# Kernel tuning notes

Hardware: AMD Instinct MI355X
Metric: run time of the kernel (lower is better)

Reference implementation:

```python
import jax, jax.numpy as jnp
import numpy as np
import math

B, S, D_IN, D_OUT, H = 2, 2048, 1024, 1024, 16
HD = D_OUT // H


def setup_inputs() -> dict:
    key = jax.random.key(0)
    ks = jax.random.split(key, 6)
    scale = 0.02
    return {
        "x": jax.random.normal(ks[0], (B, S, D_IN), dtype=jnp.float32),
        "Wq": jax.random.normal(ks[1], (D_IN, D_OUT), dtype=jnp.float32) * scale,
        "Wk": jax.random.normal(ks[2], (D_IN, D_OUT), dtype=jnp.float32) * scale,
        "Wv": jax.random.normal(ks[3], (D_IN, D_OUT), dtype=jnp.float32) * scale,
        "Wo": jax.random.normal(ks[4], (D_OUT, D_OUT), dtype=jnp.float32) * scale,
        "bo": jax.random.normal(ks[5], (D_OUT,), dtype=jnp.float32) * scale,
    }


def reference(x, Wq, Wk, Wv, Wo, bo):
    b, n, _ = x.shape
    # project and split heads -> [b, h, n, hd]
    q = (x @ Wq).reshape(b, n, H, HD).transpose(0, 2, 1, 3)
    k = (x @ Wk).reshape(b, n, H, HD).transpose(0, 2, 1, 3)
    v = (x @ Wv).reshape(b, n, H, HD).transpose(0, 2, 1, 3)
    # materialized [b, h, n, n] scores with causal mask (as in original)
    scores = jnp.einsum('bhqd,bhkd->bhqk', q, k)
    causal = jnp.tril(jnp.ones((n, n), dtype=bool))  # True = keep
    scores = jnp.where(causal, scores, -jnp.inf)
    attn = jax.nn.softmax(scores / math.sqrt(HD), axis=-1)
    ctx = jnp.einsum('bhqk,bhkd->bhqd', attn, v)
    ctx = ctx.transpose(0, 2, 1, 3).reshape(b, n, D_OUT)
    return ctx @ Wo + bo
```

## Files before the change

kernel.cpp:

```cpp
#include <hip/hip_runtime.h>
#include <hip/hip_bf16.h>
#include <math.h>

typedef __bf16 v8bf __attribute__((ext_vector_type(8)));
typedef __bf16 v4bf __attribute__((ext_vector_type(4)));
typedef short  v4s  __attribute__((ext_vector_type(4)));
typedef float  v4f  __attribute__((ext_vector_type(4)));
typedef unsigned short u16;

static_assert(sizeof(v8bf) == 16, "v8bf must be 16B");

__device__ __forceinline__ u16 f2bf(float f) {
  __hip_bfloat16 h = __float2bfloat16(f);
  return *reinterpret_cast<u16*>(&h);
}
__device__ __forceinline__ v4f mfma16(v8bf a, v8bf b, v4f c) {
  return __builtin_amdgcn_mfma_f32_16x16x32_bf16(a, b, c, 0, 0, 0);
}
__device__ __forceinline__ v4f mfma16k16(v4bf a, v4bf b, v4f c) {
#if __has_builtin(__builtin_amdgcn_mfma_f32_16x16x16_bf16)
  return __builtin_amdgcn_mfma_f32_16x16x16_bf16(a, b, c, 0, 0, 0);
#else
  union { v4bf f; v4s s; } ua, ub;
  ua.f = a; ub.f = b;
  return __builtin_amdgcn_mfma_f32_16x16x16bf16_1k(ua.s, ub.s, c, 0, 0, 0);
#endif
}
__device__ __forceinline__ void async16(const u16* g, u16* l) {
  __builtin_amdgcn_global_load_lds(
      (__attribute__((address_space(1))) void*)(void*)g,
      (__attribute__((address_space(3))) void*)l, 16, 0, 0);
}

__global__ void prep(const float* __restrict__ x, const float* __restrict__ Wq,
                     const float* __restrict__ Wk, const float* __restrict__ Wv,
                     const float* __restrict__ Wo, u16* __restrict__ Wt,
                     u16* __restrict__ xb) {
  int tx = threadIdx.x, ty = threadIdx.y;
  if (blockIdx.z == 4) {
    int bid = blockIdx.y * 32 + blockIdx.x;
    int i = (bid * 1024 + ty * 32 + tx) * 4;
    float4 v = *(const float4*)(x + i);
    ushort4 o;
    o.x = f2bf(v.x); o.y = f2bf(v.y); o.z = f2bf(v.z); o.w = f2bf(v.w);
    *(ushort4*)(xb + i) = o;
    return;
  }
  __shared__ float tile[32][33];
  const float* src = (blockIdx.z == 0) ? Wq : (blockIdx.z == 1) ? Wk : (blockIdx.z == 2) ? Wv : Wo;
  int k0 = blockIdx.x * 32, n0 = blockIdx.y * 32;
  tile[ty][tx] = src[(size_t)(k0 + ty) * 1024 + n0 + tx];
  __syncthreads();
  Wt[(size_t)(blockIdx.z * 1024 + n0 + ty) * 1024 + k0 + tx] = f2bf(tile[tx][ty]);
}

__device__ __forceinline__ void gemm_core(const u16* __restrict__ A, const u16* __restrict__ Bt,
                                          u16* sA, u16* sB, v4f acc[4][4], int bm, int bn) {
  const int t = threadIdx.x;
  const int w = t >> 6, l = t & 63;
  const int quad = l >> 4, low = l & 15;
  const int wm = (w & 1) * 64, wn = (w >> 1) * 64;
  const int rowA = bm * 128 + w * 32 + (l >> 2);
  const int rowB = bn * 128 + w * 32 + (l >> 2);
  const int col8 = (l & 3) * 8;
  u16* la = sA + w * 1024;
  u16* lb = sB + w * 1024;

  for (int kb = 0; kb < 1024; kb += 32) {
    async16(A + (size_t)rowA * 1024 + kb + col8, la);
    async16(A + (size_t)(rowA + 16) * 1024 + kb + col8, la + 512);
    async16(Bt + (size_t)rowB * 1024 + kb + col8, lb);
    async16(Bt + (size_t)(rowB + 16) * 1024 + kb + col8, lb + 512);
    __syncthreads();
    v8bf af[4], bfr[4];
#pragma unroll
    for (int i = 0; i < 4; i++)
      af[i] = *(const v8bf*)(sA + (wm + i * 16 + low) * 32 + quad * 8);
#pragma unroll
    for (int j = 0; j < 4; j++)
      bfr[j] = *(const v8bf*)(sB + (wn + j * 16 + low) * 32 + quad * 8);
#pragma unroll
    for (int i = 0; i < 4; i++)
#pragma unroll
      for (int j = 0; j < 4; j++)
        acc[i][j] = mfma16(af[i], bfr[j], acc[i][j]);
    __syncthreads();
  }
}

__global__ __launch_bounds__(256) void gemm_qkv(const u16* __restrict__ xb,
                                                const u16* __restrict__ Wt,
                                                u16* __restrict__ Qb,
                                                u16* __restrict__ Kb,
                                                u16* __restrict__ Vt) {
  __shared__ __align__(16) u16 sA[128 * 32];
  __shared__ __align__(16) u16 sB[128 * 32];
  v4f acc[4][4] = {};
  const int bm = blockIdx.x, bn = blockIdx.y;
  gemm_core(xb, Wt, sA, sB, acc, bm, bn);
  const int t = threadIdx.x, w = t >> 6, l = t & 63, quad = l >> 4, low = l & 15;
  const int wm = (w & 1) * 64, wn = (w >> 1) * 64;
  const int zone = (bn * 128) >> 10;
  const float qsc = (zone == 0) ? 0.18033688011112042f : 1.0f;
#pragma unroll
  for (int i = 0; i < 4; i++) {
    int m0 = bm * 128 + wm + i * 16 + quad * 4;
#pragma unroll
    for (int j = 0; j < 4; j++) {
      int nn = (bn * 128 + wn + j * 16 + low) & 1023;
      if (zone == 0) {
#pragma unroll
        for (int r = 0; r < 4; r++)
          Qb[(size_t)(m0 + r) * 1024 + nn] = f2bf(acc[i][j][r] * qsc);
      } else if (zone == 1) {
#pragma unroll
        for (int r = 0; r < 4; r++)
          Kb[(size_t)(m0 + r) * 1024 + nn] = f2bf(acc[i][j][r]);
      } else {
        int bb = m0 >> 11, s = m0 & 2047;
#pragma unroll
        for (int r = 0; r < 4; r++)
          Vt[(size_t)(bb * 1024 + nn) * 2048 + s + r] = f2bf(acc[i][j][r]);
      }
    }
  }
}

__global__ __launch_bounds__(256) void gemm_out(const u16* __restrict__ ctx,
                                                const u16* __restrict__ Wt,
                                                const float* __restrict__ bo,
                                                float* __restrict__ out) {
  __shared__ __align__(16) u16 sA[128 * 32];
  __shared__ __align__(16) u16 sB[64 * 32];
  const u16* Bt = Wt + (size_t)3072 * 1024;
  v4f acc[4][2] = {};
  const int bm = blockIdx.x, bn = blockIdx.y;
  const int t = threadIdx.x, w = t >> 6, l = t & 63, quad = l >> 4, low = l & 15;
  const int wm = (w & 1) * 64, wn = (w >> 1) * 32;
  const int rowA = bm * 128 + w * 32 + (l >> 2);
  const int rowB = bn * 64 + w * 16 + (l >> 2);
  const int col8 = (l & 3) * 8;
  u16* la = sA + w * 1024;
  u16* lb = sB + w * 512;

  for (int kb = 0; kb < 1024; kb += 32) {
    async16(ctx + (size_t)rowA * 1024 + kb + col8, la);
    async16(ctx + (size_t)(rowA + 16) * 1024 + kb + col8, la + 512);
    async16(Bt + (size_t)rowB * 1024 + kb + col8, lb);
    __syncthreads();
    v8bf af[4], bfr[2];
#pragma unroll
    for (int i = 0; i < 4; i++)
      af[i] = *(const v8bf*)(sA + (wm + i * 16 + low) * 32 + quad * 8);
#pragma unroll
    for (int j = 0; j < 2; j++)
      bfr[j] = *(const v8bf*)(sB + (wn + j * 16 + low) * 32 + quad * 8);
#pragma unroll
    for (int i = 0; i < 4; i++)
#pragma unroll
      for (int j = 0; j < 2; j++)
        acc[i][j] = mfma16(af[i], bfr[j], acc[i][j]);
    __syncthreads();
  }
#pragma unroll
  for (int i = 0; i < 4; i++) {
    int m0 = bm * 128 + wm + i * 16 + quad * 4;
#pragma unroll
    for (int j = 0; j < 2; j++) {
      int n = bn * 64 + wn + j * 16 + low;
      float bias = bo[n];
#pragma unroll
      for (int r = 0; r < 4; r++)
        out[(size_t)(m0 + r) * 1024 + n] = acc[i][j][r] + bias;
    }
  }
}

__global__ __launch_bounds__(256) void attn(const u16* __restrict__ Qb,
                                            const u16* __restrict__ Kb,
                                            const u16* __restrict__ Vt,
                                            u16* __restrict__ ctx) {
  __shared__ __align__(16) u16 sK[2][4096];
  __shared__ __align__(16) u16 sV[2][4096];
  const int t = threadIdx.x, w = t >> 6, l = t & 63, quad = l >> 4, low = l & 15;
  const int h = blockIdx.x, tile = 31 - blockIdx.y, b = blockIdx.z;
  const int qw = tile * 64 + w * 16;
  const int nkt = tile + 1;

  const u16* kbase = Kb + (size_t)(b * 2048) * 1024 + h * 64;
  const u16* vbase = Vt + (size_t)(b * 1024 + h * 64) * 2048;

  const int srow = l >> 3;
  const int cg = (l & 7) ^ srow;

  const u16* qrow_p = Qb + (size_t)(b * 2048 + qw + low) * 1024 + h * 64;
  v8bf qa0 = *(const v8bf*)(qrow_p + quad * 8);
  v8bf qa1 = *(const v8bf*)(qrow_p + 32 + quad * 8);

  float li = 0.f;
  v4f o[4] = {};

  {
    const u16* kg = kbase + (size_t)(w * 8 + srow) * 1024 + cg * 8;
    async16(kg, &sK[0][w * 512]);
    async16(kg + (size_t)32 * 1024, &sK[0][2048 + w * 512]);
    const u16* vg = vbase + (size_t)(w * 8 + srow) * 2048 + cg * 8;
    async16(vg, &sV[0][w * 512]);
    async16(vg + (size_t)32 * 2048, &sV[0][2048 + w * 512]);
  }

  for (int it = 0; it < nkt; it++) {
    __syncthreads();
    const int kb = it * 64;
    const int cur = it & 1;
    if (it + 1 < nkt) {
      const int nb = (it + 1) & 1;
      const u16* kg = kbase + (size_t)(kb + 64 + w * 8 + srow) * 1024 + cg * 8;
      async16(kg, &sK[nb][w * 512]);
      async16(kg + (size_t)32 * 1024, &sK[nb][2048 + w * 512]);
      const u16* vg = vbase + (size_t)(w * 8 + srow) * 2048 + kb + 64 + cg * 8;
      async16(vg, &sV[nb][w * 512]);
      async16(vg + (size_t)32 * 2048, &sV[nb][2048 + w * 512]);
    }

    v4f s[4] = {};
#pragma unroll
    for (int cf = 0; cf < 4; cf++) {
      const int key = cf * 16 + low;
      v8bf kf0 = *(const v8bf*)(&sK[cur][key * 64 + ((quad ^ (key & 7)) * 8)]);
      v8bf kf1 = *(const v8bf*)(&sK[cur][key * 64 + (((4 + quad) ^ (key & 7)) * 8)]);
      s[cf] = mfma16(kf0, qa0, s[cf]);
      s[cf] = mfma16(kf1, qa1, s[cf]);
    }

    const bool dm = (it == nkt - 1);
    const int qr = qw + low;
    v4bf pf[4];
#pragma unroll
    for (int cf = 0; cf < 4; cf++)
#pragma unroll
      for (int r = 0; r < 4; r++) {
        float e = __builtin_amdgcn_exp2f(s[cf][r]);
        if (dm && (kb + cf * 16 + quad * 4 + r > qr)) e = 0.f;
        li += e;
        pf[cf][r] = (__bf16)e;
      }

#pragma unroll
    for (int df = 0; df < 4; df++) {
      const int d = df * 16 + low;
#pragma unroll
      for (int cf = 0; cf < 4; cf++) {
        const int c = cf * 2 + (quad >> 1);
        const v4bf vf = *(const v4bf*)(&sV[cur][d * 64 + ((c ^ (d & 7)) * 8) + (quad & 1) * 4]);
        o[df] = mfma16k16(pf[cf], vf, o[df]);
      }
    }
  }

  li += __shfl_xor(li, 16);
  li += __shfl_xor(li, 32);

#pragma unroll
  for (int r = 0; r < 4; r++) {
    float lir = __shfl(li, quad * 4 + r);
    float inv = 1.f / lir;
    int row = b * 2048 + qw + quad * 4 + r;
#pragma unroll
    for (int df = 0; df < 4; df++)
      ctx[(size_t)row * 1024 + h * 64 + df * 16 + low] = f2bf(o[df][r] * inv);
  }
}

extern "C" void kernel_launch(void* const* d_in, const int* in_sizes, int n_in,
                              void* d_out, int out_size, void* d_ws, size_t ws_size,
                              hipStream_t stream) {
  const float* x  = (const float*)d_in[0];
  const float* Wq = (const float*)d_in[1];
  const float* Wk = (const float*)d_in[2];
  const float* Wv = (const float*)d_in[3];
  const float* Wo = (const float*)d_in[4];
  const float* bo = (const float*)d_in[5];
  float* out = (float*)d_out;

  char* ws = (char*)d_ws;
  u16* xb  = (u16*)(ws);
  u16* Wt  = (u16*)(ws + 8ull * 1024 * 1024);
  u16* Qb  = (u16*)(ws + 16ull * 1024 * 1024);
  u16* Kb  = (u16*)(ws + 24ull * 1024 * 1024);
  u16* Vt  = (u16*)(ws + 32ull * 1024 * 1024);
  u16* ctx = (u16*)(ws + 40ull * 1024 * 1024);

  prep<<<dim3(32, 32, 5), dim3(32, 32, 1), 0, stream>>>(x, Wq, Wk, Wv, Wo, Wt, xb);
  gemm_qkv<<<dim3(32, 24, 1), dim3(256, 1, 1), 0, stream>>>(xb, Wt, Qb, Kb, Vt);
  attn<<<dim3(16, 32, 2), dim3(256, 1, 1), 0, stream>>>(Qb, Kb, Vt, ctx);
  gemm_out<<<dim3(32, 16, 1), dim3(256, 1, 1), 0, stream>>>(ctx, Wt, bo, out);
}
```

Baseline: 178.9 us.

## Pair causal tiles per block, deepen K/V prefetch, XCD-aware head mapping

The attention kernel now gives each block two query tiles, tile 31-tp and tile tp, so every block does the same amount of causal work. The block index is remapped so that blocks sharing a batch-head pair land on the same XCD, which should improve L2 reuse of K/V. The K/V shared-memory ring grows from 2 to 4 buffers with a prefetch distance of 2, explicit vmcnt waits and raw barriers, and MFMA sections get raised s_setprio. Costs are double the LDS use, which may lower occupancy, and fragile hand-written waitcnt logic. The grid drops to 512 blocks.

```diff
diff --git a/kernel.cpp b/kernel.cpp
--- a/kernel.cpp
+++ b/kernel.cpp
@@ -180,12 +180,15 @@
                                             const u16* __restrict__ Kb,
                                             const u16* __restrict__ Vt,
                                             u16* __restrict__ ctx) {
-  __shared__ __align__(16) u16 sK[2][4096];
-  __shared__ __align__(16) u16 sV[2][4096];
+  __shared__ __align__(16) u16 sK[4][4096];
+  __shared__ __align__(16) u16 sV[4][4096];
   const int t = threadIdx.x, w = t >> 6, l = t & 63, quad = l >> 4, low = l & 15;
-  const int h = blockIdx.x, tile = 31 - blockIdx.y, b = blockIdx.z;
-  const int qw = tile * 64 + w * 16;
-  const int nkt = tile + 1;
+
+  const int bid = blockIdx.x;
+  const int xcd = bid & 7, slot = bid >> 3;
+  const int pair = xcd * 4 + (slot & 3);
+  const int tp = slot >> 2;
+  const int b = pair >> 4, h = pair & 15;
 
   const u16* kbase = Kb + (size_t)(b * 2048) * 1024 + h * 64;
   const u16* vbase = Vt + (size_t)(b * 1024 + h * 64) * 2048;
@@ -193,82 +196,99 @@
   const int srow = l >> 3;
   const int cg = (l & 7) ^ srow;
 
-  const u16* qrow_p = Qb + (size_t)(b * 2048 + qw + low) * 1024 + h * 64;
-  v8bf qa0 = *(const v8bf*)(qrow_p + quad * 8);
-  v8bf qa1 = *(const v8bf*)(qrow_p + 32 + quad * 8);
-
-  float li = 0.f;
-  v4f o[4] = {};
-
-  {
-    const u16* kg = kbase + (size_t)(w * 8 + srow) * 1024 + cg * 8;
-    async16(kg, &sK[0][w * 512]);
-    async16(kg + (size_t)32 * 1024, &sK[0][2048 + w * 512]);
-    const u16* vg = vbase + (size_t)(w * 8 + srow) * 2048 + cg * 8;
-    async16(vg, &sV[0][w * 512]);
-    async16(vg + (size_t)32 * 2048, &sV[0][2048 + w * 512]);
-  }
-
-  for (int it = 0; it < nkt; it++) {
-    __syncthreads();
-    const int kb = it * 64;
-    const int cur = it & 1;
-    if (it + 1 < nkt) {
-      const int nb = (it + 1) & 1;
-      const u16* kg = kbase + (size_t)(kb + 64 + w * 8 + srow) * 1024 + cg * 8;
-      async16(kg, &sK[nb][w * 512]);
-      async16(kg + (size_t)32 * 1024, &sK[nb][2048 + w * 512]);
-      const u16* vg = vbase + (size_t)(w * 8 + srow) * 2048 + kb + 64 + cg * 8;
-      async16(vg, &sV[nb][w * 512]);
-      async16(vg + (size_t)32 * 2048, &sV[nb][2048 + w * 512]);
-    }
-
-    v4f s[4] = {};
-#pragma unroll
-    for (int cf = 0; cf < 4; cf++) {
-      const int key = cf * 16 + low;
-      v8bf kf0 = *(const v8bf*)(&sK[cur][key * 64 + ((quad ^ (key & 7)) * 8)]);
-      v8bf kf1 = *(const v8bf*)(&sK[cur][key * 64 + (((4 + quad) ^ (key & 7)) * 8)]);
-      s[cf] = mfma16(kf0, qa0, s[cf]);
-      s[cf] = mfma16(kf1, qa1, s[cf]);
-    }
-
-    const bool dm = (it == nkt - 1);
-    const int qr = qw + low;
-    v4bf pf[4];
-#pragma unroll
-    for (int cf = 0; cf < 4; cf++)
-#pragma unroll
-      for (int r = 0; r < 4; r++) {
-        float e = __builtin_amdgcn_exp2f(s[cf][r]);
-        if (dm && (kb + cf * 16 + quad * 4 + r > qr)) e = 0.f;
-        li += e;
-        pf[cf][r] = (__bf16)e;
+  auto STAGE = [&](int tt, int bi) {
+    const int kb = tt * 64;
+    const u16* kg = kbase + (size_t)(kb + w * 8 + srow) * 1024 + cg * 8;
+    async16(kg, &sK[bi][w * 512]);
+    async16(kg + (size_t)32 * 1024, &sK[bi][2048 + w * 512]);
+    const u16* vg = vbase + (size_t)(w * 8 + srow) * 2048 + kb + cg * 8;
+    async16(vg, &sV[bi][w * 512]);
+    async16(vg + (size_t)32 * 2048, &sV[bi][2048 + w * 512]);
+  };
+
+  for (int ph = 0; ph < 2; ++ph) {
+    const int tile = ph ? tp : 31 - tp;
+    const int nkt = tile + 1;
+    const int qw = tile * 64 + w * 16;
+
+    if (ph) {
+      asm volatile("s_waitcnt lgkmcnt(0)" ::: "memory");
+      __builtin_amdgcn_s_barrier();
+    }
+
+    const u16* qrow_p = Qb + (size_t)(b * 2048 + qw + low) * 1024 + h * 64;
+    v8bf qa0 = *(const v8bf*)(qrow_p + quad * 8);
+    v8bf qa1 = *(const v8bf*)(qrow_p + 32 + quad * 8);
+    asm volatile("" ::: "memory");
+
+    float li = 0.f;
+    v4f o[4] = {};
+
+    STAGE(0, 0);
+    if (nkt > 1) STAGE(1, 1);
+
+    for (int it = 0; it < nkt; ++it) {
+      const int bi = it & 3;
+      if (it + 2 < nkt) STAGE(it + 2, (it + 2) & 3);
+      asm volatile("s_waitcnt lgkmcnt(0)" ::: "memory");
+      const int c = nkt - 1 - it;
+      if (c >= 2)      asm volatile("s_waitcnt vmcnt(8)" ::: "memory");
+      else if (c == 1) asm volatile("s_waitcnt vmcnt(4)" ::: "memory");
+      else             asm volatile("s_waitcnt vmcnt(0)" ::: "memory");
+      __builtin_amdgcn_s_barrier();
+
+      const int kb = it * 64;
+      v4f s[4] = {};
+      __builtin_amdgcn_s_setprio(1);
+#pragma unroll
+      for (int cf = 0; cf < 4; cf++) {
+        const int key = cf * 16 + low;
+        v8bf kf0 = *(const v8bf*)(&sK[bi][key * 64 + ((quad ^ (key & 7)) * 8)]);
+        v8bf kf1 = *(const v8bf*)(&sK[bi][key * 64 + (((4 + quad) ^ (key & 7)) * 8)]);
+        s[cf] = mfma16(kf0, qa0, s[cf]);
+        s[cf] = mfma16(kf1, qa1, s[cf]);
       }
-
-#pragma unroll
-    for (int df = 0; df < 4; df++) {
-      const int d = df * 16 + low;
-#pragma unroll
-      for (int cf = 0; cf < 4; cf++) {
-        const int c = cf * 2 + (quad >> 1);
-        const v4bf vf = *(const v4bf*)(&sV[cur][d * 64 + ((c ^ (d & 7)) * 8) + (quad & 1) * 4]);
-        o[df] = mfma16k16(pf[cf], vf, o[df]);
+      __builtin_amdgcn_s_setprio(0);
+
+      const bool dm = (it == nkt - 1);
+      const int qr = qw + low;
+      v4bf pf[4];
+#pragma unroll
+      for (int cf = 0; cf < 4; cf++)
+#pragma unroll
+        for (int r = 0; r < 4; r++) {
+          float e = __builtin_amdgcn_exp2f(s[cf][r]);
+          if (dm && (kb + cf * 16 + quad * 4 + r > qr)) e = 0.f;
+          li += e;
+          pf[cf][r] = (__bf16)e;
+        }
+
+      __builtin_amdgcn_s_setprio(1);
+#pragma unroll
+      for (int df = 0; df < 4; df++) {
+        const int d = df * 16 + low;
+#pragma unroll
+        for (int cf = 0; cf < 4; cf++) {
+          const int c2 = cf * 2 + (quad >> 1);
+          const v4bf vf = *(const v4bf*)(&sV[bi][d * 64 + ((c2 ^ (d & 7)) * 8) + (quad & 1) * 4]);
+          o[df] = mfma16k16(pf[cf], vf, o[df]);
+        }
       }
-    }
-  }
-
-  li += __shfl_xor(li, 16);
-  li += __shfl_xor(li, 32);
-
-#pragma unroll
-  for (int r = 0; r < 4; r++) {
-    float lir = __shfl(li, quad * 4 + r);
-    float inv = 1.f / lir;
-    int row = b * 2048 + qw + quad * 4 + r;
-#pragma unroll
-    for (int df = 0; df < 4; df++)
-      ctx[(size_t)row * 1024 + h * 64 + df * 16 + low] = f2bf(o[df][r] * inv);
+      __builtin_amdgcn_s_setprio(0);
+    }
+
+    li += __shfl_xor(li, 16);
+    li += __shfl_xor(li, 32);
+
+#pragma unroll
+    for (int r = 0; r < 4; r++) {
+      float lir = __shfl(li, quad * 4 + r);
+      float inv = 1.f / lir;
+      int row = b * 2048 + qw + quad * 4 + r;
+#pragma unroll
+      for (int df = 0; df < 4; df++)
+        ctx[(size_t)row * 1024 + h * 64 + df * 16 + low] = f2bf(o[df][r] * inv);
+    }
   }
 }
 
@@ -293,6 +313,6 @@
 
   prep<<<dim3(32, 32, 5), dim3(32, 32, 1), 0, stream>>>(x, Wq, Wk, Wv, Wo, Wt, xb);
   gemm_qkv<<<dim3(32, 24, 1), dim3(256, 1, 1), 0, stream>>>(xb, Wt, Qb, Kb, Vt);
-  attn<<<dim3(16, 32, 2), dim3(256, 1, 1), 0, stream>>>(Qb, Kb, Vt, ctx);
+  attn<<<dim3(512, 1, 1), dim3(256, 1, 1), 0, stream>>>(Qb, Kb, Vt, ctx);
   gemm_out<<<dim3(32, 16, 1), dim3(256, 1, 1), 0, stream>>>(ctx, Wt, bo, out);
 }
```

Result: no change. 175.5 us (-1.9%).
